# Kernel optimization log

Hardware: AMD Instinct MI355X
Metric: run time of the kernel (lower is better)

Reference implementation:

```python
import jax, jax.numpy as jnp
import numpy as np

N_NODES = 50000
N_EDGES = 800000
IN_DIM, HID_DIM, OUT_DIM = 256, 128, 64


def gcn_conv(x, edge_index, W, b):
    """PyG GCNConv: out = D^{-1/2} (A + I) D^{-1/2} (x @ W) + b."""
    n = x.shape[0]
    loops = jnp.arange(n, dtype=edge_index.dtype)
    src = jnp.concatenate([edge_index[0], loops])  # message source j
    dst = jnp.concatenate([edge_index[1], loops])  # aggregation target i
    ones = jnp.ones(src.shape[0], dtype=x.dtype)
    deg = jax.ops.segment_sum(ones, dst, num_segments=n)  # >= 1 (self-loops)
    dinv = jax.lax.rsqrt(deg)
    norm = dinv[src] * dinv[dst]                    # [E+N]
    h = x @ W                                       # [N, out] GEMM first (PyG order)
    msg = h[src] * norm[:, None]                    # gather + scale
    out = jax.ops.segment_sum(msg, dst, num_segments=n)  # scatter-add
    return out + b


def setup_inputs() -> dict:
    key = jax.random.key(0)
    k1, k2, k3, k4, k5 = jax.random.split(key, 5)
    x = jax.random.normal(k1, (N_NODES, IN_DIM), dtype=jnp.float32)
    edge_index = jax.random.randint(k2, (2, N_EDGES), 0, N_NODES, dtype=jnp.int64)
    # Glorot-ish init for weights, zero bias (PyG defaults)
    W1 = jax.random.normal(k3, (IN_DIM, HID_DIM), dtype=jnp.float32) / np.sqrt(IN_DIM)
    b1 = jnp.zeros((HID_DIM,), dtype=jnp.float32)
    W2 = jax.random.normal(k4, (HID_DIM, OUT_DIM), dtype=jnp.float32) / np.sqrt(HID_DIM)
    b2 = jnp.zeros((OUT_DIM,), dtype=jnp.float32)
    return {"x": x, "edge_index": edge_index, "W1": W1, "b1": b1, "W2": W2, "b2": b2}


def reference(x, edge_index, W1, b1, W2, b2):
    h = jax.nn.relu(gcn_conv(x, edge_index, W1, b1))
    return gcn_conv(h, edge_index, W2, b2)
```

## Files before the change

### kernel.cpp

```cpp
#include <hip/hip_runtime.h>

#define N_NODES 50000
#define N_EDGES 800000
#define IN_DIM 256
#define HID_DIM 128
#define OUT_DIM 64
#define CAP 64

#define K_BINS 256
#define NPB 196
#define BINCAP 4096
#define CHUNK 4096
#define N_BINWG 196

typedef __bf16 bf16x8 __attribute__((ext_vector_type(8)));
typedef float f32x4 __attribute__((ext_vector_type(4)));
typedef unsigned short u16x8 __attribute__((ext_vector_type(8)));
typedef unsigned short ushort_t;
typedef unsigned int uint_t;

__device__ __forceinline__ ushort_t f2bf(float f) {
    uint_t u = __float_as_uint(f);
    return (ushort_t)((u + 0x7fffu + ((u >> 16) & 1u)) >> 16);
}
__device__ __forceinline__ float bf_lo(uint_t u) { return __uint_as_float(u << 16); }
__device__ __forceinline__ float bf_hi(uint_t u) { return __uint_as_float(u & 0xffff0000u); }

__global__ __launch_bounds__(256) void k_init(const float* __restrict__ W1,
                                              ushort_t* __restrict__ w1t,
                                              const float* __restrict__ W2,
                                              ushort_t* __restrict__ w2t) {
    const int bid = blockIdx.x;
    const int t = threadIdx.x;
    if (bid < 128) {
        int id = bid * 256 + t;
        int k = id >> 7, c = id & 127;
        w1t[c * IN_DIM + k] = f2bf(W1[id]);
    } else {
        int id = (bid - 128) * 256 + t;
        int k = id >> 6, c = id & 63;
        w2t[c * HID_DIM + k] = f2bf(W2[id]);
    }
}

__global__ __launch_bounds__(256) void k_bin(const int* __restrict__ srcs,
                                             const int* __restrict__ dsts,
                                             int* __restrict__ bin_cur,
                                             uint_t* __restrict__ binbuf) {
    __shared__ int lcnt[K_BINS];
    __shared__ int lbase[K_BINS];
    const int t = threadIdx.x;
    lcnt[t] = 0;
    __syncthreads();
    const int start = blockIdx.x * CHUNK;
    int b_[16]; int p_[16]; uint_t rec_[16];
#pragma unroll
    for (int k = 0; k < 16; ++k) {
        int e = start + t + k * 256;
        bool ok = (e < N_EDGES);
        int d = ok ? dsts[e] : 0;
        int s = ok ? srcs[e] : 0;
        int b = d / NPB;
        b_[k] = ok ? b : -1;
        p_[k] = ok ? atomicAdd(&lcnt[b], 1) : 0;
        rec_[k] = (uint_t)s | ((uint_t)(d - b * NPB) << 16);
    }
    __syncthreads();
    lbase[t] = atomicAdd(&bin_cur[t], lcnt[t]);
    __syncthreads();
#pragma unroll
    for (int k = 0; k < 16; ++k) {
        if (b_[k] >= 0) {
            int pos = lbase[b_[k]] + p_[k];
            if (pos < BINCAP) binbuf[(size_t)b_[k] * BINCAP + pos] = rec_[k];
        }
    }
}

__global__ __launch_bounds__(256) void k_fill(const int* __restrict__ bin_cur,
                                              const uint_t* __restrict__ binbuf,
                                              ushort_t* __restrict__ es,
                                              float* __restrict__ dinv,
                                              int* __restrict__ ndeg) {
    __shared__ int cnt[NPB];
    __shared__ __align__(16) ushort_t pay[NPB][CAP];
    const int b = blockIdx.x, t = threadIdx.x;
    if (t < NPB) cnt[t] = 0;
    __syncthreads();
    const int n = min(bin_cur[b], BINCAP);
    const uint_t* rec = binbuf + (size_t)b * BINCAP;
    for (int e = t; e < n; e += 256) {
        uint_t r = rec[e];
        int dl = r >> 16;
        int p = atomicAdd(&cnt[dl], 1);
        if (p < CAP) pay[dl][p] = (ushort_t)(r & 0xffffu);
    }
    __syncthreads();
    uint4* gdst = (uint4*)(es + (size_t)b * NPB * CAP);
    const uint4* lsrc = (const uint4*)&pay[0][0];
    for (int i = t; i < NPB * CAP / 8; i += 256) gdst[i] = lsrc[i];
    if (t < NPB) {
        int node = b * NPB + t;
        if (node < N_NODES) {
            int deg = cnt[t];
            dinv[node] = rsqrtf((float)(deg + 1));
            ndeg[node] = min(deg, CAP);
        }
    }
}

__global__ __launch_bounds__(64) void k_gemm1(const float* __restrict__ x,
                                              const ushort_t* __restrict__ w1t,
                                              ushort_t* __restrict__ hb) {
    const int lane = threadIdx.x;
    const int l15 = lane & 15, quad = lane >> 4;
    const int row = blockIdx.x * 16 + l15;
    f32x4 acc[8];
#pragma unroll
    for (int n = 0; n < 8; ++n) acc[n] = (f32x4){0.f, 0.f, 0.f, 0.f};
    const float* xrow = x + (size_t)row * IN_DIM + quad * 8;
    const ushort_t* wbase = w1t + quad * 8;
#pragma unroll
    for (int t = 0; t < 8; ++t) {
        const float4* xp = (const float4*)(xrow + t * 32);
        float4 f0 = xp[0], f1 = xp[1];
        u16x8 au;
        au[0] = f2bf(f0.x); au[1] = f2bf(f0.y); au[2] = f2bf(f0.z); au[3] = f2bf(f0.w);
        au[4] = f2bf(f1.x); au[5] = f2bf(f1.y); au[6] = f2bf(f1.z); au[7] = f2bf(f1.w);
        bf16x8 a = __builtin_bit_cast(bf16x8, au);
#pragma unroll
        for (int n = 0; n < 8; ++n) {
            bf16x8 b = *(const bf16x8*)(wbase + (n * 16 + l15) * IN_DIM + t * 32);
            acc[n] = __builtin_amdgcn_mfma_f32_16x16x32_bf16(a, b, acc[n], 0, 0, 0);
        }
    }
    ushort_t* hrow = hb + ((size_t)blockIdx.x * 16 + quad * 4) * HID_DIM + l15;
#pragma unroll
    for (int n = 0; n < 8; ++n)
#pragma unroll
        for (int r = 0; r < 4; ++r)
            hrow[(size_t)r * HID_DIM + n * 16] = f2bf(acc[n][r]);
}

__global__ __launch_bounds__(256) void k_agg1(const ushort_t* __restrict__ hb,
                                              const int* __restrict__ ndeg,
                                              const float* __restrict__ dinv,
                                              const ushort_t* __restrict__ es,
                                              const float* __restrict__ b,
                                              ushort_t* __restrict__ hrelu) {
    const int i = blockIdx.x * 4 + (threadIdx.x >> 6);
    const int lane = threadIdx.x & 63;
    const float dv = dinv[i];
    const int n = ndeg[i];
    int   sj = 0;
    float nmj = 0.f;
    if (lane < n) {
        sj = (int)es[i * CAP + lane];
        nmj = dinv[sj] * dv;
    }
    uint_t u = *(const uint_t*)(hb + (size_t)i * HID_DIM + 2 * lane);
    float a0 = bf_lo(u) * dv * dv;
    float a1 = bf_hi(u) * dv * dv;
    int j = 0;
    for (; j + 8 <= n; j += 8) {
        int s0 = __shfl(sj, j),     s1 = __shfl(sj, j + 1);
        int s2 = __shfl(sj, j + 2), s3 = __shfl(sj, j + 3);
        int s4 = __shfl(sj, j + 4), s5 = __shfl(sj, j + 5);
        int s6 = __shfl(sj, j + 6), s7 = __shfl(sj, j + 7);
        float m0 = __shfl(nmj, j),     m1 = __shfl(nmj, j + 1);
        float m2 = __shfl(nmj, j + 2), m3 = __shfl(nmj, j + 3);
        float m4 = __shfl(nmj, j + 4), m5 = __shfl(nmj, j + 5);
        float m6 = __shfl(nmj, j + 6), m7 = __shfl(nmj, j + 7);
        uint_t v0 = *(const uint_t*)(hb + (size_t)s0 * HID_DIM + 2 * lane);
        uint_t v1 = *(const uint_t*)(hb + (size_t)s1 * HID_DIM + 2 * lane);
        uint_t v2 = *(const uint_t*)(hb + (size_t)s2 * HID_DIM + 2 * lane);
        uint_t v3 = *(const uint_t*)(hb + (size_t)s3 * HID_DIM + 2 * lane);
        uint_t v4 = *(const uint_t*)(hb + (size_t)s4 * HID_DIM + 2 * lane);
        uint_t v5 = *(const uint_t*)(hb + (size_t)s5 * HID_DIM + 2 * lane);
        uint_t v6 = *(const uint_t*)(hb + (size_t)s6 * HID_DIM + 2 * lane);
        uint_t v7 = *(const uint_t*)(hb + (size_t)s7 * HID_DIM + 2 * lane);
        a0 += bf_lo(v0) * m0 + bf_lo(v1) * m1 + bf_lo(v2) * m2 + bf_lo(v3) * m3
            + bf_lo(v4) * m4 + bf_lo(v5) * m5 + bf_lo(v6) * m6 + bf_lo(v7) * m7;
        a1 += bf_hi(v0) * m0 + bf_hi(v1) * m1 + bf_hi(v2) * m2 + bf_hi(v3) * m3
            + bf_hi(v4) * m4 + bf_hi(v5) * m5 + bf_hi(v6) * m6 + bf_hi(v7) * m7;
    }
    for (; j + 4 <= n; j += 4) {
        int s0 = __shfl(sj, j),     s1 = __shfl(sj, j + 1);
        int s2 = __shfl(sj, j + 2), s3 = __shfl(sj, j + 3);
        float m0 = __shfl(nmj, j),     m1 = __shfl(nmj, j + 1);
        float m2 = __shfl(nmj, j + 2), m3 = __shfl(nmj, j + 3);
        uint_t v0 = *(const uint_t*)(hb + (size_t)s0 * HID_DIM + 2 * lane);
        uint_t v1 = *(const uint_t*)(hb + (size_t)s1 * HID_DIM + 2 * lane);
        uint_t v2 = *(const uint_t*)(hb + (size_t)s2 * HID_DIM + 2 * lane);
        uint_t v3 = *(const uint_t*)(hb + (size_t)s3 * HID_DIM + 2 * lane);
        a0 += bf_lo(v0) * m0 + bf_lo(v1) * m1 + bf_lo(v2) * m2 + bf_lo(v3) * m3;
        a1 += bf_hi(v0) * m0 + bf_hi(v1) * m1 + bf_hi(v2) * m2 + bf_hi(v3) * m3;
    }
    for (; j < n; ++j) {
        int s = __shfl(sj, j);
        float nm = __shfl(nmj, j);
        uint_t v = *(const uint_t*)(hb + (size_t)s * HID_DIM + 2 * lane);
        a0 += bf_lo(v) * nm;
        a1 += bf_hi(v) * nm;
    }
    float v0 = a0 + b[2 * lane];     v0 = v0 > 0.f ? v0 : 0.f;
    float v1 = a1 + b[2 * lane + 1]; v1 = v1 > 0.f ? v1 : 0.f;
    *(uint_t*)(hrelu + (size_t)i * HID_DIM + 2 * lane) = ((uint_t)f2bf(v1) << 16) | f2bf(v0);
}

__global__ __launch_bounds__(64) void k_gemm2(const ushort_t* __restrict__ hrelu,
                                              const ushort_t* __restrict__ w2t,
                                              ushort_t* __restrict__ h2) {
    const int lane = threadIdx.x;
    const int l15 = lane & 15, quad = lane >> 4;
    const int row = blockIdx.x * 16 + l15;
    f32x4 acc[4];
#pragma unroll
    for (int n = 0; n < 4; ++n) acc[n] = (f32x4){0.f, 0.f, 0.f, 0.f};
    const ushort_t* arow = hrelu + (size_t)row * HID_DIM + quad * 8;
    const ushort_t* wbase = w2t + quad * 8;
#pragma unroll
    for (int t = 0; t < 4; ++t) {
        bf16x8 a = *(const bf16x8*)(arow + t * 32);
#pragma unroll
        for (int n = 0; n < 4; ++n) {
            bf16x8 b = *(const bf16x8*)(wbase + (n * 16 + l15) * HID_DIM + t * 32);
            acc[n] = __builtin_amdgcn_mfma_f32_16x16x32_bf16(a, b, acc[n], 0, 0, 0);
        }
    }
    ushort_t* orow = h2 + ((size_t)blockIdx.x * 16 + quad * 4) * OUT_DIM + l15;
#pragma unroll
    for (int n = 0; n < 4; ++n)
#pragma unroll
        for (int r = 0; r < 4; ++r)
            orow[(size_t)r * OUT_DIM + n * 16] = f2bf(acc[n][r]);
}

__global__ __launch_bounds__(256) void k_agg2(const ushort_t* __restrict__ h2,
                                              const int* __restrict__ ndeg,
                                              const float* __restrict__ dinv,
                                              const ushort_t* __restrict__ es,
                                              const float* __restrict__ b,
                                              float* __restrict__ out) {
    const int i = blockIdx.x * 4 + (threadIdx.x >> 6);
    const int lane = threadIdx.x & 63;
    const float dv = dinv[i];
    const int n = ndeg[i];
    int   sj = 0;
    float nmj = 0.f;
    if (lane < n) {
        sj = (int)es[i * CAP + lane];
        nmj = dinv[sj] * dv;
    }
    float acc = __uint_as_float(((uint_t)h2[(size_t)i * OUT_DIM + lane]) << 16) * dv * dv;
    int j = 0;
    for (; j + 8 <= n; j += 8) {
        int s0 = __shfl(sj, j),     s1 = __shfl(sj, j + 1);
        int s2 = __shfl(sj, j + 2), s3 = __shfl(sj, j + 3);
        int s4 = __shfl(sj, j + 4), s5 = __shfl(sj, j + 5);
        int s6 = __shfl(sj, j + 6), s7 = __shfl(sj, j + 7);
        float m0 = __shfl(nmj, j),     m1 = __shfl(nmj, j + 1);
        float m2 = __shfl(nmj, j + 2), m3 = __shfl(nmj, j + 3);
        float m4 = __shfl(nmj, j + 4), m5 = __shfl(nmj, j + 5);
        float m6 = __shfl(nmj, j + 6), m7 = __shfl(nmj, j + 7);
        float v0 = __uint_as_float(((uint_t)h2[(size_t)s0 * OUT_DIM + lane]) << 16);
        float v1 = __uint_as_float(((uint_t)h2[(size_t)s1 * OUT_DIM + lane]) << 16);
        float v2 = __uint_as_float(((uint_t)h2[(size_t)s2 * OUT_DIM + lane]) << 16);
        float v3 = __uint_as_float(((uint_t)h2[(size_t)s3 * OUT_DIM + lane]) << 16);
        float v4 = __uint_as_float(((uint_t)h2[(size_t)s4 * OUT_DIM + lane]) << 16);
        float v5 = __uint_as_float(((uint_t)h2[(size_t)s5 * OUT_DIM + lane]) << 16);
        float v6 = __uint_as_float(((uint_t)h2[(size_t)s6 * OUT_DIM + lane]) << 16);
        float v7 = __uint_as_float(((uint_t)h2[(size_t)s7 * OUT_DIM + lane]) << 16);
        acc += v0 * m0 + v1 * m1 + v2 * m2 + v3 * m3 + v4 * m4 + v5 * m5 + v6 * m6 + v7 * m7;
    }
    for (; j + 4 <= n; j += 4) {
        int s0 = __shfl(sj, j),     s1 = __shfl(sj, j + 1);
        int s2 = __shfl(sj, j + 2), s3 = __shfl(sj, j + 3);
        float m0 = __shfl(nmj, j),     m1 = __shfl(nmj, j + 1);
        float m2 = __shfl(nmj, j + 2), m3 = __shfl(nmj, j + 3);
        float v0 = __uint_as_float(((uint_t)h2[(size_t)s0 * OUT_DIM + lane]) << 16);
        float v1 = __uint_as_float(((uint_t)h2[(size_t)s1 * OUT_DIM + lane]) << 16);
        float v2 = __uint_as_float(((uint_t)h2[(size_t)s2 * OUT_DIM + lane]) << 16);
        float v3 = __uint_as_float(((uint_t)h2[(size_t)s3 * OUT_DIM + lane]) << 16);
        acc += v0 * m0 + v1 * m1 + v2 * m2 + v3 * m3;
    }
    for (; j < n; ++j) {
        int s = __shfl(sj, j);
        float nm = __shfl(nmj, j);
        acc += __uint_as_float(((uint_t)h2[(size_t)s * OUT_DIM + lane]) << 16) * nm;
    }
    out[(size_t)i * OUT_DIM + lane] = acc + b[lane];
}

extern "C" void kernel_launch(void* const* d_in, const int* in_sizes, int n_in,
                              void* d_out, int out_size, void* d_ws, size_t ws_size,
                              hipStream_t stream) {
    const float* x   = (const float*)d_in[0];
    const int*   ei  = (const int*)d_in[1];
    const float* W1  = (const float*)d_in[2];
    const float* b1  = (const float*)d_in[3];
    const float* W2  = (const float*)d_in[4];
    const float* b2  = (const float*)d_in[5];
    float* out = (float*)d_out;

    const int* srcs = ei;
    const int* dsts = ei + N_EDGES;

    char* ws = (char*)d_ws;
    size_t o = 0;
    auto alloc = [&](size_t bytes) { void* p = ws + o; o = (o + bytes + 511) & ~size_t(511); return p; };
    int*      bin_cur = (int*)   alloc(K_BINS * 4);
    float*    dinv  = (float*)   alloc(N_NODES * 4);
    int*      ndeg  = (int*)     alloc(N_NODES * 4);
    ushort_t* es    = (ushort_t*)alloc((size_t)K_BINS * NPB * CAP * 2);
    uint_t*   binbuf= (uint_t*)  alloc((size_t)K_BINS * BINCAP * 4);
    ushort_t* w1t   = (ushort_t*)alloc((size_t)IN_DIM * HID_DIM * 2);
    ushort_t* w2t   = (ushort_t*)alloc((size_t)HID_DIM * OUT_DIM * 2);
    ushort_t* hb    = (ushort_t*)alloc((size_t)N_NODES * HID_DIM * 2);
    ushort_t* hrelu = (ushort_t*)alloc((size_t)N_NODES * HID_DIM * 2);
    ushort_t* h2    = (ushort_t*)alloc((size_t)N_NODES * OUT_DIM * 2);

    hipMemsetAsync(bin_cur, 0, K_BINS * 4, stream);
    k_init  <<<160, 256, 0, stream>>>(W1, w1t, W2, w2t);
    k_bin   <<<N_BINWG, 256, 0, stream>>>(srcs, dsts, bin_cur, binbuf);
    k_fill  <<<K_BINS, 256, 0, stream>>>(bin_cur, binbuf, es, dinv, ndeg);
    k_gemm1 <<<N_NODES / 16, 64, 0, stream>>>(x, w1t, hb);
    k_agg1  <<<N_NODES / 4, 256, 0, stream>>>(hb, ndeg, dinv, es, b1, hrelu);
    k_gemm2 <<<N_NODES / 16, 64, 0, stream>>>(hrelu, w2t, h2);
    k_agg2  <<<N_NODES / 4, 256, 0, stream>>>(h2, ndeg, dinv, es, b2, out);
}
```

Baseline: 214.6 us.

## Split feature matrices into 32-column planes to shrink gather working set

Stores hidden and second-layer features in column-sliced planes of 32 bf16 values per node, and launches the aggregation kernels once per plane. Each wave gathers 8 neighbors at a time, with 16 lanes per neighbor covering 64-byte rows, then reduces across lane groups. The aim is to keep each plane's gather working set small enough to stay cache-resident and to raise memory-level parallelism. In exchange it adds more blocks, cross-lane reductions and repeated loading of the index/degree data per plane.

```diff
diff --git a/kernel.cpp b/kernel.cpp
--- a/kernel.cpp
+++ b/kernel.cpp
@@ -6,12 +6,15 @@
 #define HID_DIM 128
 #define OUT_DIM 64
 #define CAP 64
+#define NPAD 50176
 
 #define K_BINS 256
 #define NPB 196
 #define BINCAP 4096
 #define CHUNK 4096
 #define N_BINWG 196
+
+#define N_NB 12500
 
 typedef __bf16 bf16x8 __attribute__((ext_vector_type(8)));
 typedef float f32x4 __attribute__((ext_vector_type(4)));
@@ -111,7 +114,7 @@
 
 __global__ __launch_bounds__(64) void k_gemm1(const float* __restrict__ x,
                                               const ushort_t* __restrict__ w1t,
-                                              ushort_t* __restrict__ hb) {
+                                              ushort_t* __restrict__ hbp) {
     const int lane = threadIdx.x;
     const int l15 = lane & 15, quad = lane >> 4;
     const int row = blockIdx.x * 16 + l15;
@@ -134,22 +137,27 @@
             acc[n] = __builtin_amdgcn_mfma_f32_16x16x32_bf16(a, b, acc[n], 0, 0, 0);
         }
     }
-    ushort_t* hrow = hb + ((size_t)blockIdx.x * 16 + quad * 4) * HID_DIM + l15;
-#pragma unroll
-    for (int n = 0; n < 8; ++n)
+    const int orow0 = blockIdx.x * 16 + quad * 4;
+#pragma unroll
+    for (int n = 0; n < 8; ++n) {
+        ushort_t* pl = hbp + ((size_t)(n >> 1) * NPAD + orow0) * 32 + (n & 1) * 16 + l15;
 #pragma unroll
         for (int r = 0; r < 4; ++r)
-            hrow[(size_t)r * HID_DIM + n * 16] = f2bf(acc[n][r]);
-}
-
-__global__ __launch_bounds__(256) void k_agg1(const ushort_t* __restrict__ hb,
+            pl[(size_t)r * 32] = f2bf(acc[n][r]);
+    }
+}
+
+__global__ __launch_bounds__(256) void k_agg1(const ushort_t* __restrict__ hbp,
                                               const int* __restrict__ ndeg,
                                               const float* __restrict__ dinv,
                                               const ushort_t* __restrict__ es,
                                               const float* __restrict__ b,
-                                              ushort_t* __restrict__ hrelu) {
-    const int i = blockIdx.x * 4 + (threadIdx.x >> 6);
+                                              ushort_t* __restrict__ hrelup) {
+    const int q = blockIdx.x / N_NB;
+    const int i = (blockIdx.x - q * N_NB) * 4 + (threadIdx.x >> 6);
     const int lane = threadIdx.x & 63;
+    const int g = lane >> 4;
+    const int ch = lane & 15;
     const float dv = dinv[i];
     const int n = ndeg[i];
     int   sj = 0;
@@ -158,92 +166,71 @@
         sj = (int)es[i * CAP + lane];
         nmj = dinv[sj] * dv;
     }
-    uint_t u = *(const uint_t*)(hb + (size_t)i * HID_DIM + 2 * lane);
-    float a0 = bf_lo(u) * dv * dv;
-    float a1 = bf_hi(u) * dv * dv;
-    int j = 0;
-    for (; j + 8 <= n; j += 8) {
-        int s0 = __shfl(sj, j),     s1 = __shfl(sj, j + 1);
-        int s2 = __shfl(sj, j + 2), s3 = __shfl(sj, j + 3);
-        int s4 = __shfl(sj, j + 4), s5 = __shfl(sj, j + 5);
-        int s6 = __shfl(sj, j + 6), s7 = __shfl(sj, j + 7);
-        float m0 = __shfl(nmj, j),     m1 = __shfl(nmj, j + 1);
-        float m2 = __shfl(nmj, j + 2), m3 = __shfl(nmj, j + 3);
-        float m4 = __shfl(nmj, j + 4), m5 = __shfl(nmj, j + 5);
-        float m6 = __shfl(nmj, j + 6), m7 = __shfl(nmj, j + 7);
-        uint_t v0 = *(const uint_t*)(hb + (size_t)s0 * HID_DIM + 2 * lane);
-        uint_t v1 = *(const uint_t*)(hb + (size_t)s1 * HID_DIM + 2 * lane);
-        uint_t v2 = *(const uint_t*)(hb + (size_t)s2 * HID_DIM + 2 * lane);
-        uint_t v3 = *(const uint_t*)(hb + (size_t)s3 * HID_DIM + 2 * lane);
-        uint_t v4 = *(const uint_t*)(hb + (size_t)s4 * HID_DIM + 2 * lane);
-        uint_t v5 = *(const uint_t*)(hb + (size_t)s5 * HID_DIM + 2 * lane);
-        uint_t v6 = *(const uint_t*)(hb + (size_t)s6 * HID_DIM + 2 * lane);
-        uint_t v7 = *(const uint_t*)(hb + (size_t)s7 * HID_DIM + 2 * lane);
-        a0 += bf_lo(v0) * m0 + bf_lo(v1) * m1 + bf_lo(v2) * m2 + bf_lo(v3) * m3
-            + bf_lo(v4) * m4 + bf_lo(v5) * m5 + bf_lo(v6) * m6 + bf_lo(v7) * m7;
-        a1 += bf_hi(v0) * m0 + bf_hi(v1) * m1 + bf_hi(v2) * m2 + bf_hi(v3) * m3
-            + bf_hi(v4) * m4 + bf_hi(v5) * m5 + bf_hi(v6) * m6 + bf_hi(v7) * m7;
-    }
-    for (; j + 4 <= n; j += 4) {
-        int s0 = __shfl(sj, j),     s1 = __shfl(sj, j + 1);
-        int s2 = __shfl(sj, j + 2), s3 = __shfl(sj, j + 3);
-        float m0 = __shfl(nmj, j),     m1 = __shfl(nmj, j + 1);
-        float m2 = __shfl(nmj, j + 2), m3 = __shfl(nmj, j + 3);
-        uint_t v0 = *(const uint_t*)(hb + (size_t)s0 * HID_DIM + 2 * lane);
-        uint_t v1 = *(const uint_t*)(hb + (size_t)s1 * HID_DIM + 2 * lane);
-        uint_t v2 = *(const uint_t*)(hb + (size_t)s2 * HID_DIM + 2 * lane);
-        uint_t v3 = *(const uint_t*)(hb + (size_t)s3 * HID_DIM + 2 * lane);
-        a0 += bf_lo(v0) * m0 + bf_lo(v1) * m1 + bf_lo(v2) * m2 + bf_lo(v3) * m3;
-        a1 += bf_hi(v0) * m0 + bf_hi(v1) * m1 + bf_hi(v2) * m2 + bf_hi(v3) * m3;
-    }
-    for (; j < n; ++j) {
-        int s = __shfl(sj, j);
-        float nm = __shfl(nmj, j);
-        uint_t v = *(const uint_t*)(hb + (size_t)s * HID_DIM + 2 * lane);
-        a0 += bf_lo(v) * nm;
-        a1 += bf_hi(v) * nm;
-    }
-    float v0 = a0 + b[2 * lane];     v0 = v0 > 0.f ? v0 : 0.f;
-    float v1 = a1 + b[2 * lane + 1]; v1 = v1 > 0.f ? v1 : 0.f;
-    *(uint_t*)(hrelu + (size_t)i * HID_DIM + 2 * lane) = ((uint_t)f2bf(v1) << 16) | f2bf(v0);
-}
-
-__global__ __launch_bounds__(64) void k_gemm2(const ushort_t* __restrict__ hrelu,
+    const ushort_t* hq = hbp + (size_t)q * NPAD * 32;
+    float accA = 0.f, accB = 0.f;
+    for (int j = 0; j < n; j += 8) {
+        int   sA = __shfl(sj, j + g);
+        int   sB = __shfl(sj, j + 4 + g);
+        float mA = __shfl(nmj, j + g);
+        float mB = __shfl(nmj, j + 4 + g);
+        uint_t vA = *(const uint_t*)(hq + (size_t)sA * 32 + 2 * ch);
+        uint_t vB = *(const uint_t*)(hq + (size_t)sB * 32 + 2 * ch);
+        accA += bf_lo(vA) * mA + bf_lo(vB) * mB;
+        accB += bf_hi(vA) * mA + bf_hi(vB) * mB;
+    }
+    accA += __shfl_xor(accA, 16); accA += __shfl_xor(accA, 32);
+    accB += __shfl_xor(accB, 16); accB += __shfl_xor(accB, 32);
+    if (lane < 16) {
+        uint_t u = *(const uint_t*)(hq + (size_t)i * 32 + 2 * ch);
+        float v0 = accA + bf_lo(u) * dv * dv + b[q * 32 + 2 * ch];
+        float v1 = accB + bf_hi(u) * dv * dv + b[q * 32 + 2 * ch + 1];
+        v0 = v0 > 0.f ? v0 : 0.f;
+        v1 = v1 > 0.f ? v1 : 0.f;
+        *(uint_t*)(hrelup + ((size_t)q * NPAD + i) * 32 + 2 * ch) =
+            ((uint_t)f2bf(v1) << 16) | f2bf(v0);
+    }
+}
+
+__global__ __launch_bounds__(64) void k_gemm2(const ushort_t* __restrict__ hrelup,
                                               const ushort_t* __restrict__ w2t,
-                                              ushort_t* __restrict__ h2) {
+                                              ushort_t* __restrict__ h2p) {
     const int lane = threadIdx.x;
     const int l15 = lane & 15, quad = lane >> 4;
     const int row = blockIdx.x * 16 + l15;
     f32x4 acc[4];
 #pragma unroll
     for (int n = 0; n < 4; ++n) acc[n] = (f32x4){0.f, 0.f, 0.f, 0.f};
-    const ushort_t* arow = hrelu + (size_t)row * HID_DIM + quad * 8;
     const ushort_t* wbase = w2t + quad * 8;
 #pragma unroll
     for (int t = 0; t < 4; ++t) {
-        bf16x8 a = *(const bf16x8*)(arow + t * 32);
+        bf16x8 a = *(const bf16x8*)(hrelup + ((size_t)t * NPAD + row) * 32 + quad * 8);
 #pragma unroll
         for (int n = 0; n < 4; ++n) {
             bf16x8 b = *(const bf16x8*)(wbase + (n * 16 + l15) * HID_DIM + t * 32);
             acc[n] = __builtin_amdgcn_mfma_f32_16x16x32_bf16(a, b, acc[n], 0, 0, 0);
         }
     }
-    ushort_t* orow = h2 + ((size_t)blockIdx.x * 16 + quad * 4) * OUT_DIM + l15;
-#pragma unroll
-    for (int n = 0; n < 4; ++n)
+    const int orow0 = blockIdx.x * 16 + quad * 4;
+#pragma unroll
+    for (int n = 0; n < 4; ++n) {
+        ushort_t* pl = h2p + ((size_t)(n >> 1) * NPAD + orow0) * 32 + (n & 1) * 16 + l15;
 #pragma unroll
         for (int r = 0; r < 4; ++r)
-            orow[(size_t)r * OUT_DIM + n * 16] = f2bf(acc[n][r]);
-}
-
-__global__ __launch_bounds__(256) void k_agg2(const ushort_t* __restrict__ h2,
+            pl[(size_t)r * 32] = f2bf(acc[n][r]);
+    }
+}
+
+__global__ __launch_bounds__(256) void k_agg2(const ushort_t* __restrict__ h2p,
                                               const int* __restrict__ ndeg,
                                               const float* __restrict__ dinv,
                                               const ushort_t* __restrict__ es,
                                               const float* __restrict__ b,
                                               float* __restrict__ out) {
-    const int i = blockIdx.x * 4 + (threadIdx.x >> 6);
+    const int h = blockIdx.x / N_NB;
+    const int i = (blockIdx.x - h * N_NB) * 4 + (threadIdx.x >> 6);
     const int lane = threadIdx.x & 63;
+    const int g = lane >> 4;
+    const int ch = lane & 15;
     const float dv = dinv[i];
     const int n = ndeg[i];
     int   sj = 0;
@@ -252,44 +239,27 @@
         sj = (int)es[i * CAP + lane];
         nmj = dinv[sj] * dv;
     }
-    float acc = __uint_as_float(((uint_t)h2[(size_t)i * OUT_DIM + lane]) << 16) * dv * dv;
-    int j = 0;
-    for (; j + 8 <= n; j += 8) {
-        int s0 = __shfl(sj, j),     s1 = __shfl(sj, j + 1);
-        int s2 = __shfl(sj, j + 2), s3 = __shfl(sj, j + 3);
-        int s4 = __shfl(sj, j + 4), s5 = __shfl(sj, j + 5);
-        int s6 = __shfl(sj, j + 6), s7 = __shfl(sj, j + 7);
-        float m0 = __shfl(nmj, j),     m1 = __shfl(nmj, j + 1);
-        float m2 = __shfl(nmj, j + 2), m3 = __shfl(nmj, j + 3);
-        float m4 = __shfl(nmj, j + 4), m5 = __shfl(nmj, j + 5);
-        float m6 = __shfl(nmj, j + 6), m7 = __shfl(nmj, j + 7);
-        float v0 = __uint_as_float(((uint_t)h2[(size_t)s0 * OUT_DIM + lane]) << 16);
-        float v1 = __uint_as_float(((uint_t)h2[(size_t)s1 * OUT_DIM + lane]) << 16);
-        float v2 = __uint_as_float(((uint_t)h2[(size_t)s2 * OUT_DIM + lane]) << 16);
-        float v3 = __uint_as_float(((uint_t)h2[(size_t)s3 * OUT_DIM + lane]) << 16);
-        float v4 = __uint_as_float(((uint_t)h2[(size_t)s4 * OUT_DIM + lane]) << 16);
-        float v5 = __uint_as_float(((uint_t)h2[(size_t)s5 * OUT_DIM + lane]) << 16);
-        float v6 = __uint_as_float(((uint_t)h2[(size_t)s6 * OUT_DIM + lane]) << 16);
-        float v7 = __uint_as_float(((uint_t)h2[(size_t)s7 * OUT_DIM + lane]) << 16);
-        acc += v0 * m0 + v1 * m1 + v2 * m2 + v3 * m3 + v4 * m4 + v5 * m5 + v6 * m6 + v7 * m7;
-    }
-    for (; j + 4 <= n; j += 4) {
-        int s0 = __shfl(sj, j),     s1 = __shfl(sj, j + 1);
-        int s2 = __shfl(sj, j + 2), s3 = __shfl(sj, j + 3);
-        float m0 = __shfl(nmj, j),     m1 = __shfl(nmj, j + 1);
-        float m2 = __shfl(nmj, j + 2), m3 = __shfl(nmj, j + 3);
-        float v0 = __uint_as_float(((uint_t)h2[(size_t)s0 * OUT_DIM + lane]) << 16);
-        float v1 = __uint_as_float(((uint_t)h2[(size_t)s1 * OUT_DIM + lane]) << 16);
-        float v2 = __uint_as_float(((uint_t)h2[(size_t)s2 * OUT_DIM + lane]) << 16);
-        float v3 = __uint_as_float(((uint_t)h2[(size_t)s3 * OUT_DIM + lane]) << 16);
-        acc += v0 * m0 + v1 * m1 + v2 * m2 + v3 * m3;
-    }
-    for (; j < n; ++j) {
-        int s = __shfl(sj, j);
-        float nm = __shfl(nmj, j);
-        acc += __uint_as_float(((uint_t)h2[(size_t)s * OUT_DIM + lane]) << 16) * nm;
-    }
-    out[(size_t)i * OUT_DIM + lane] = acc + b[lane];
+    const ushort_t* hq = h2p + (size_t)h * NPAD * 32;
+    float accA = 0.f, accB = 0.f;
+    for (int j = 0; j < n; j += 8) {
+        int   sA = __shfl(sj, j + g);
+        int   sB = __shfl(sj, j + 4 + g);
+        float mA = __shfl(nmj, j + g);
+        float mB = __shfl(nmj, j + 4 + g);
+        uint_t vA = *(const uint_t*)(hq + (size_t)sA * 32 + 2 * ch);
+        uint_t vB = *(const uint_t*)(hq + (size_t)sB * 32 + 2 * ch);
+        accA += bf_lo(vA) * mA + bf_lo(vB) * mB;
+        accB += bf_hi(vA) * mA + bf_hi(vB) * mB;
+    }
+    accA += __shfl_xor(accA, 16); accA += __shfl_xor(accA, 32);
+    accB += __shfl_xor(accB, 16); accB += __shfl_xor(accB, 32);
+    if (lane < 16) {
+        uint_t u = *(const uint_t*)(hq + (size_t)i * 32 + 2 * ch);
+        float2 r;
+        r.x = accA + bf_lo(u) * dv * dv + b[h * 32 + 2 * ch];
+        r.y = accB + bf_hi(u) * dv * dv + b[h * 32 + 2 * ch + 1];
+        *(float2*)(out + (size_t)i * OUT_DIM + h * 32 + 2 * ch) = r;
+    }
 }
 
 extern "C" void kernel_launch(void* const* d_in, const int* in_sizes, int n_in,
@@ -316,16 +286,16 @@
     uint_t*   binbuf= (uint_t*)  alloc((size_t)K_BINS * BINCAP * 4);
     ushort_t* w1t   = (ushort_t*)alloc((size_t)IN_DIM * HID_DIM * 2);
     ushort_t* w2t   = (ushort_t*)alloc((size_t)HID_DIM * OUT_DIM * 2);
-    ushort_t* hb    = (ushort_t*)alloc((size_t)N_NODES * HID_DIM * 2);
-    ushort_t* hrelu = (ushort_t*)alloc((size_t)N_NODES * HID_DIM * 2);
-    ushort_t* h2    = (ushort_t*)alloc((size_t)N_NODES * OUT_DIM * 2);
+    ushort_t* hbp   = (ushort_t*)alloc((size_t)4 * NPAD * 32 * 2);
+    ushort_t* hrelup= (ushort_t*)alloc((size_t)4 * NPAD * 32 * 2);
+    ushort_t* h2p   = (ushort_t*)alloc((size_t)2 * NPAD * 32 * 2);
 
     hipMemsetAsync(bin_cur, 0, K_BINS * 4, stream);
     k_init  <<<160, 256, 0, stream>>>(W1, w1t, W2, w2t);
     k_bin   <<<N_BINWG, 256, 0, stream>>>(srcs, dsts, bin_cur, binbuf);
     k_fill  <<<K_BINS, 256, 0, stream>>>(bin_cur, binbuf, es, dinv, ndeg);
-    k_gemm1 <<<N_NODES / 16, 64, 0, stream>>>(x, w1t, hb);
-    k_agg1  <<<N_NODES / 4, 256, 0, stream>>>(hb, ndeg, dinv, es, b1, hrelu);
-    k_gemm2 <<<N_NODES / 16, 64, 0, stream>>>(hrelu, w2t, h2);
-    k_agg2  <<<N_NODES / 4, 256, 0, stream>>>(h2, ndeg, dinv, es, b2, out);
-}
+    k_gemm1 <<<N_NODES / 16, 64, 0, stream>>>(x, w1t, hbp);
+    k_agg1  <<<4 * N_NB, 256, 0, stream>>>(hbp, ndeg, dinv, es, b1, hrelup);
+    k_gemm2 <<<N_NODES / 16, 64, 0, stream>>>(hrelup, w2t, h2p);
+    k_agg2  <<<2 * N_NB, 256, 0, stream>>>(h2p, ndeg, dinv, es, b2, out);
+}
```

New measurement: 258.7 us. 1.21x slower.
